# Performance work log

Measured on AMD Instinct MI355X. Metric: run time of the kernel, lower is better.

## Reference

```python
import jax, jax.numpy as jnp
import numpy as np

EMBED = 1024
HEADS = 16
HEAD_DIM = EMBED // HEADS


def setup_inputs() -> dict:
    key = jax.random.key(0)
    ks = jax.random.split(key, 5)
    x = jax.random.normal(ks[0], (4, 2048, EMBED), dtype=jnp.float32)
    s = 1.0 / np.sqrt(EMBED)
    W_qkv = jax.random.normal(ks[1], (EMBED, 3 * EMBED), dtype=jnp.float32) * s
    b_qkv = jnp.zeros((3 * EMBED,), dtype=jnp.float32)
    W_proj = jax.random.normal(ks[2], (EMBED, EMBED), dtype=jnp.float32) * s
    b_proj = jnp.zeros((EMBED,), dtype=jnp.float32)
    return {"x": x, "W_qkv": W_qkv, "b_qkv": b_qkv, "W_proj": W_proj, "b_proj": b_proj}


def reference(x, W_qkv, b_qkv, W_proj, b_proj):
    B, S, E = x.shape
    scale = 1.0 / np.sqrt(HEAD_DIM)
    qkv = x @ W_qkv + b_qkv                      # [B,S,3E]
    qkv = qkv.reshape(B, S, 3, HEADS, HEAD_DIM)
    q, k, v = qkv[:, :, 0], qkv[:, :, 1], qkv[:, :, 2]   # [B,S,H,D]
    scores = jnp.einsum('bshd,bthd->bhst', q, k) * scale  # [B,H,S,S]
    attn = jax.nn.softmax(scores, axis=-1)
    out = jnp.einsum('bhst,bthd->bshd', attn, v)          # [B,S,H,D]
    out = out.reshape(B, S, E)
    return out @ W_proj + b_proj
```

## Files before the change

kernel.cpp:

```cpp
#include <hip/hip_runtime.h>
#include <math.h>

#define EMBED 1024
#define HEADS 16
#define HD    64
#define SEQ   2048
#define BATCH 4
#define ROWS  (BATCH * SEQ)

typedef _Float16 f16;
typedef __attribute__((ext_vector_type(8))) _Float16 f16x8;
typedef __attribute__((ext_vector_type(4))) _Float16 f16x4;
typedef __attribute__((ext_vector_type(2))) _Float16 f16x2;
typedef __attribute__((ext_vector_type(4))) float    fx4;

typedef __attribute__((address_space(3))) char  lds_char;
typedef __attribute__((address_space(1))) const char glb_char;

#define SCALE_Q 0.18033688011112042f

#define BAR_LGKM()  asm volatile("s_waitcnt lgkmcnt(0)\n\ts_barrier" ::: "memory")
#define BAR_VM8()   asm volatile("s_waitcnt vmcnt(8)\n\ts_barrier" ::: "memory")
#define BAR_VM0()   asm volatile("s_waitcnt vmcnt(0)\n\ts_barrier" ::: "memory")

__global__ __launch_bounds__(256) void prep(const float* __restrict__ x,
                                            f16* __restrict__ x_h,
                                            const float* __restrict__ Wqkv,
                                            f16* __restrict__ Wqt,
                                            const float* __restrict__ Wproj,
                                            f16* __restrict__ Wpt) {
    const int blk = blockIdx.x;
    if (blk < 8192) {
        const int i = (blk * 256 + threadIdx.x) * 4;
        const float4 v = *(const float4*)(x + i);
        f16x4 o = {(f16)v.x, (f16)v.y, (f16)v.z, (f16)v.w};
        *(f16x4*)(x_h + i) = o;
        return;
    }
    __shared__ float t[32][33];
    const float* W;
    f16* Wt;
    int N, bx, by;
    if (blk < 8192 + 3072) {
        const int b2 = blk - 8192;
        W = Wqkv; Wt = Wqt; N = 3072; bx = b2 % 96; by = b2 / 96;
    } else {
        const int b2 = blk - 8192 - 3072;
        W = Wproj; Wt = Wpt; N = 1024; bx = b2 % 32; by = b2 / 32;
    }
    const int tx = threadIdx.x & 31, ty = threadIdx.x >> 5;
    const int k0 = by * 32, n0 = bx * 32;
    #pragma unroll
    for (int i = 0; i < 4; i++)
        t[ty + i * 8][tx] = W[(size_t)(k0 + ty + i * 8) * N + n0 + tx];
    __syncthreads();
    #pragma unroll
    for (int i = 0; i < 4; i++)
        Wt[(size_t)(n0 + ty + i * 8) * 1024 + k0 + tx] = (f16)t[tx][ty + i * 8];
}

template <int MODE>
__global__ __launch_bounds__(256) void gemm_f16k(const f16* __restrict__ A,
                                                 const f16* __restrict__ Bt,
                                                 const float* __restrict__ bias,
                                                 float* __restrict__ Cf,
                                                 f16* __restrict__ qH,
                                                 f16* __restrict__ kH,
                                                 f16* __restrict__ vT,
                                                 int M, int N, int K) {
    constexpr int TEL = 128 * 64;
    __shared__ alignas(16) f16 smem[4 * TEL];

    f16 (*As0)[64] = (f16(*)[64])(smem);
    f16 (*As1)[64] = (f16(*)[64])(smem + TEL);
    f16 (*Bs0)[64] = (f16(*)[64])(smem + 2 * TEL);
    f16 (*Bs1)[64] = (f16(*)[64])(smem + 3 * TEL);
    lds_char* a0b = (lds_char*)smem;
    lds_char* a1b = (lds_char*)smem + 2 * TEL;
    lds_char* b0b = (lds_char*)smem + 4 * TEL;
    lds_char* b1b = (lds_char*)smem + 6 * TEL;

    const int tid  = threadIdx.x;
    const int wave = tid >> 6;
    const int lane = tid & 63;
    const int quad = lane >> 4;
    const int l16  = lane & 15;

    const int nwg  = gridDim.x * gridDim.y;
    const int flat = blockIdx.y * gridDim.x + blockIdx.x;
    const int swz  = (flat & 7) * (nwg >> 3) + (flat >> 3);
    const int bx   = swz % gridDim.x;
    const int by   = swz / gridDim.x;
    const int m0   = by * 128;
    const int n0   = bx * 128;
    const int wm   = wave & 1;
    const int wn   = wave >> 1;

    fx4 acc[4][4];
    #pragma unroll
    for (int i = 0; i < 4; i++)
        #pragma unroll
        for (int j = 0; j < 4; j++)
            acc[i][j] = (fx4){0.f, 0.f, 0.f, 0.f};

    const int srow = lane >> 3;
    const int sjl  = ((lane & 7) ^ (srow & 7)) * 8;
    auto STAGE = [&](lds_char* asb, lds_char* bsb, int k0) {
        #pragma unroll
        for (int it = 0; it < 4; it++) {
            const int g = it * 4 + wave;
            const int r = g * 8 + srow;
            __builtin_amdgcn_global_load_lds(
                (glb_char*)(A + (size_t)(m0 + r) * K + k0 + sjl),
                asb + g * 1024, 16, 0, 0);
            __builtin_amdgcn_global_load_lds(
                (glb_char*)(Bt + (size_t)(n0 + r) * K + k0 + sjl),
                bsb + g * 1024, 16, 0, 0);
        }
    };

    const int NT = K >> 6;

    auto ITER = [&](f16 (*As)[64], f16 (*Bs)[64],
                    lds_char* asb, lds_char* bsb, int t) {
        f16x8 af0[4], af1[4], bf0[4], bf1[4];
        #pragma unroll
        for (int i = 0; i < 4; i++) {
            const int ra = wm * 64 + i * 16 + l16;
            const int rb = wn * 64 + i * 16 + l16;
            af0[i] = *(const f16x8*)&As[ra][((0 + quad) ^ (ra & 7)) * 8];
            af1[i] = *(const f16x8*)&As[ra][((4 + quad) ^ (ra & 7)) * 8];
            bf0[i] = *(const f16x8*)&Bs[rb][((0 + quad) ^ (rb & 7)) * 8];
            bf1[i] = *(const f16x8*)&Bs[rb][((4 + quad) ^ (rb & 7)) * 8];
        }
        BAR_LGKM();
        const bool more = (t + 2 < NT);
        if (more) STAGE(asb, bsb, (t + 2) * 64);
        __builtin_amdgcn_s_setprio(1);
        #pragma unroll
        for (int i = 0; i < 4; i++)
            #pragma unroll
            for (int j = 0; j < 4; j++) {
                acc[i][j] = __builtin_amdgcn_mfma_f32_16x16x32_f16(af0[i], bf0[j], acc[i][j], 0, 0, 0);
                acc[i][j] = __builtin_amdgcn_mfma_f32_16x16x32_f16(af1[i], bf1[j], acc[i][j], 0, 0, 0);
            }
        __builtin_amdgcn_s_setprio(0);
        if (more) BAR_VM8(); else BAR_VM0();
    };

    STAGE(a0b, b0b, 0);
    STAGE(a1b, b1b, 64);
    BAR_VM8();

    for (int t = 0; t < NT; t += 2) {
        ITER(As0, Bs0, a0b, b0b, t);
        ITER(As1, Bs1, a1b, b1b, t + 1);
    }

    const int region = (MODE == 1) ? (n0 >> 10) : 0;

    if (MODE == 1 && region == 2) {
        const int b  = m0 >> 11;
        const int s0 = m0 & 2047;
        #pragma unroll
        for (int i = 0; i < 4; i++) {
            #pragma unroll
            for (int j = 0; j < 4; j++) {
                const int nloc = wn * 64 + j * 16 + l16;
                const float bn = bias[n0 + nloc];
                #pragma unroll
                for (int r = 0; r < 4; r++) {
                    const int sloc = wm * 64 + i * 16 + quad * 4 + r;
                    const int sp   = (sloc & ~31) | ((sloc & 15) << 1) | ((sloc >> 4) & 1);
                    const int phys = (sp >> 3) ^ (nloc & 15);
                    smem[nloc * 128 + phys * 8 + (sp & 7)] = (f16)(acc[i][j][r] + bn);
                }
            }
        }
        __syncthreads();
        const int nl = tid >> 1;
        const int hf = tid & 1;
        const int np0 = n0 - 2048;
        f16* dst = vT + ((size_t)(b * 16 + ((np0 + nl) >> 6)) * HD + (nl & 63)) * SEQ
                      + s0 + hf * 64;
        #pragma unroll
        for (int ch = 0; ch < 8; ch++) {
            const int lc   = hf * 8 + ch;
            const int phys = lc ^ (nl & 15);
            const f16x8 v  = *(const f16x8*)&smem[nl * 128 + phys * 8];
            *(f16x8*)(dst + ch * 8) = v;
        }
        return;
    }

    #pragma unroll
    for (int i = 0; i < 4; i++) {
        const int mb = m0 + wm * 64 + i * 16 + quad * 4;
        #pragma unroll
        for (int j = 0; j < 4; j++) {
            const int n  = n0 + wn * 64 + j * 16 + l16;
            const float bn = bias[n];
            #pragma unroll
            for (int r = 0; r < 4; r++) {
                const int m = mb + r;
                const float v = acc[i][j][r] + bn;
                if (MODE == 0) {
                    Cf[(size_t)m * N + n] = v;
                } else {
                    const int b = m >> 11, s = m & 2047;
                    if (region == 0) {
                        qH[(size_t)m * EMBED + n] = (f16)(v * SCALE_Q);
                    } else {
                        const int np = n - 1024, hh = np >> 6, d = np & 63;
                        kH[(((size_t)(b * 16 + hh) * SEQ + s) << 6) + d] = (f16)v;
                    }
                }
            }
        }
    }
}

__global__ __launch_bounds__(256, 4) void attn_mfma(const f16* __restrict__ qH,
                                                    const f16* __restrict__ kH,
                                                    const f16* __restrict__ vT,
                                                    f16* __restrict__ ctx) {
    __shared__ alignas(16) f16 Ks[64 * 64];
    __shared__ alignas(16) f16 Vt[64 * 64];
    __shared__ alignas(16) f16 Pl[4][2][16 * 64];

    const int tid  = threadIdx.x;
    const int wave = tid >> 6;
    const int lane = tid & 63;
    const int quad = lane >> 4;
    const int l16  = lane & 15;

    const int bid = (int)blockIdx.x;
    const int swz = (bid & 7) * 128 + (bid >> 3);
    const int qb = swz & 15;
    const int bh = swz >> 4;
    const int h  = bh & 15;
    const int b  = bh >> 4;
    const int q0 = qb * 128 + wave * 32;

    const f16* kB = kH + (size_t)bh * SEQ * HD;
    const f16* vB = vT + (size_t)bh * HD * SEQ;

    f16x8 qf[2][2];
    #pragma unroll
    for (int s = 0; s < 2; s++) {
        const f16* qp = qH + (size_t)(b * SEQ + q0 + s * 16 + l16) * EMBED + h * HD;
        #pragma unroll
        for (int c = 0; c < 2; c++)
            qf[s][c] = *(const f16x8*)(qp + c * 32 + quad * 8);
    }

    fx4 o[2][4];
    fx4 ls[2];
    #pragma unroll
    for (int s = 0; s < 2; s++) {
        ls[s] = (fx4){0.f, 0.f, 0.f, 0.f};
        #pragma unroll
        for (int dc = 0; dc < 4; dc++)
            o[s][dc] = (fx4){0.f, 0.f, 0.f, 0.f};
    }

    f16x8 ones8;
    #pragma unroll
    for (int j = 0; j < 8; j++) ones8[j] = (f16)1.0f;

    lds_char* ksb = (lds_char*)&Ks[0];
    lds_char* vsb = (lds_char*)&Vt[0];

    auto STAGE_K = [&](int kb) {
        #pragma unroll
        for (int it = 0; it < 2; it++) {
            const int g  = wave * 2 + it;
            const int c  = g * 64 + lane;
            const int r  = c >> 3;
            const int jl = (c & 7) ^ (r & 7);
            __builtin_amdgcn_global_load_lds(
                (glb_char*)(kB + (size_t)(kb * 64 + r) * HD + jl * 8),
                ksb + g * 1024, 16, 0, 0);
        }
    };
    auto STAGE_V = [&](int kb) {
        #pragma unroll
        for (int it = 0; it < 2; it++) {
            const int g  = wave * 2 + it;
            const int c  = g * 64 + lane;
            const int r  = c >> 3;
            const int jl = (c & 7) ^ (r & 7);
            __builtin_amdgcn_global_load_lds(
                (glb_char*)(vB + (size_t)r * SEQ + kb * 64 + jl * 8),
                vsb + g * 1024, 16, 0, 0);
        }
    };

    STAGE_K(0);
    STAGE_V(0);
    __syncthreads();

    for (int kb = 0; kb < SEQ / 64; kb++) {
        fx4 st0[4], st1[4];
        __builtin_amdgcn_s_setprio(1);
        #pragma unroll
        for (int t = 0; t < 4; t++) {
            const int row = l16 + 16 * t;
            const f16x8 kt0 = *(const f16x8*)&Ks[(row * 8 + ((0 + quad) ^ (row & 7))) * 8];
            const f16x8 kt1 = *(const f16x8*)&Ks[(row * 8 + ((4 + quad) ^ (row & 7))) * 8];
            fx4 z = {0.f, 0.f, 0.f, 0.f};
            st0[t] = __builtin_amdgcn_mfma_f32_16x16x32_f16(qf[0][0], kt0, z, 0, 0, 0);
            st0[t] = __builtin_amdgcn_mfma_f32_16x16x32_f16(qf[0][1], kt1, st0[t], 0, 0, 0);
            st1[t] = __builtin_amdgcn_mfma_f32_16x16x32_f16(qf[1][0], kt0, z, 0, 0, 0);
            st1[t] = __builtin_amdgcn_mfma_f32_16x16x32_f16(qf[1][1], kt1, st1[t], 0, 0, 0);
        }
        __builtin_amdgcn_s_setprio(0);

        #pragma unroll
        for (int g = 0; g < 2; g++)
            #pragma unroll
            for (int r = 0; r < 4; r++) {
                const int row = quad * 4 + r;
                const int cc  = (g * 4 + (l16 >> 2)) ^ (row & 7);
                {
                    const float pa = __builtin_amdgcn_exp2f(st0[2 * g][r]);
                    const float pb = __builtin_amdgcn_exp2f(st0[2 * g + 1][r]);
                    const f16x2 pk = __builtin_bit_cast(f16x2, __builtin_amdgcn_cvt_pkrtz(pa, pb));
                    *(f16x2*)&Pl[wave][0][row * 64 + cc * 8 + (l16 & 3) * 2] = pk;
                }
                {
                    const float pa = __builtin_amdgcn_exp2f(st1[2 * g][r]);
                    const float pb = __builtin_amdgcn_exp2f(st1[2 * g + 1][r]);
                    const f16x2 pk = __builtin_bit_cast(f16x2, __builtin_amdgcn_cvt_pkrtz(pa, pb));
                    *(f16x2*)&Pl[wave][1][row * 64 + cc * 8 + (l16 & 3) * 2] = pk;
                }
            }

        __syncthreads();
        if (kb + 1 < SEQ / 64) STAGE_K(kb + 1);

        const f16x8 pf00 = *(const f16x8*)&Pl[wave][0][l16 * 64 + ((0 + quad) ^ (l16 & 7)) * 8];
        const f16x8 pf01 = *(const f16x8*)&Pl[wave][0][l16 * 64 + ((4 + quad) ^ (l16 & 7)) * 8];
        const f16x8 pf10 = *(const f16x8*)&Pl[wave][1][l16 * 64 + ((0 + quad) ^ (l16 & 7)) * 8];
        const f16x8 pf11 = *(const f16x8*)&Pl[wave][1][l16 * 64 + ((4 + quad) ^ (l16 & 7)) * 8];
        __builtin_amdgcn_s_setprio(1);
        #pragma unroll
        for (int dc = 0; dc < 4; dc++) {
            const int row = 16 * dc + l16;
            const f16x8 vf0 = *(const f16x8*)&Vt[(row * 8 + ((0 + quad) ^ (row & 7))) * 8];
            const f16x8 vf1 = *(const f16x8*)&Vt[(row * 8 + ((4 + quad) ^ (row & 7))) * 8];
            o[0][dc] = __builtin_amdgcn_mfma_f32_16x16x32_f16(pf00, vf0, o[0][dc], 0, 0, 0);
            o[0][dc] = __builtin_amdgcn_mfma_f32_16x16x32_f16(pf01, vf1, o[0][dc], 0, 0, 0);
            o[1][dc] = __builtin_amdgcn_mfma_f32_16x16x32_f16(pf10, vf0, o[1][dc], 0, 0, 0);
            o[1][dc] = __builtin_amdgcn_mfma_f32_16x16x32_f16(pf11, vf1, o[1][dc], 0, 0, 0);
        }
        ls[0] = __builtin_amdgcn_mfma_f32_16x16x32_f16(pf00, ones8, ls[0], 0, 0, 0);
        ls[0] = __builtin_amdgcn_mfma_f32_16x16x32_f16(pf01, ones8, ls[0], 0, 0, 0);
        ls[1] = __builtin_amdgcn_mfma_f32_16x16x32_f16(pf10, ones8, ls[1], 0, 0, 0);
        ls[1] = __builtin_amdgcn_mfma_f32_16x16x32_f16(pf11, ones8, ls[1], 0, 0, 0);
        __builtin_amdgcn_s_setprio(0);

        __syncthreads();
        if (kb + 1 < SEQ / 64) STAGE_V(kb + 1);
    }

    #pragma unroll
    for (int s = 0; s < 2; s++) {
        #pragma unroll
        for (int r = 0; r < 4; r++) {
            const float inv = 1.0f / ls[s][r];
            const int q = q0 + s * 16 + quad * 4 + r;
            f16* dst = ctx + (size_t)(b * SEQ + q) * EMBED + h * HD;
            #pragma unroll
            for (int dc = 0; dc < 4; dc++)
                dst[dc * 16 + l16] = (f16)(o[s][dc][r] * inv);
        }
    }
}

extern "C" void kernel_launch(void* const* d_in, const int* in_sizes, int n_in,
                              void* d_out, int out_size, void* d_ws, size_t ws_size,
                              hipStream_t stream) {
    const float* x     = (const float*)d_in[0];
    const float* Wqkv  = (const float*)d_in[1];
    const float* bqkv  = (const float*)d_in[2];
    const float* Wproj = (const float*)d_in[3];
    const float* bproj = (const float*)d_in[4];
    float* out = (float*)d_out;

    f16* x_h = (f16*)d_ws;
    f16* qHb = x_h + (size_t)ROWS * EMBED;
    f16* kHb = qHb + (size_t)ROWS * EMBED;
    f16* vTb = kHb + (size_t)ROWS * EMBED;
    f16* ctx = vTb + (size_t)ROWS * EMBED;
    f16* Wqt = ctx + (size_t)ROWS * EMBED;
    f16* Wpt = Wqt + (size_t)3 * EMBED * EMBED;

    prep<<<dim3(12288), dim3(256), 0, stream>>>(x, x_h, Wqkv, Wqt, Wproj, Wpt);

    gemm_f16k<1><<<dim3(3 * EMBED / 128, ROWS / 128), dim3(256), 0, stream>>>(
        x_h, Wqt, bqkv, nullptr, qHb, kHb, vTb, ROWS, 3 * EMBED, EMBED);

    attn_mfma<<<dim3(64 * 16), dim3(256), 0, stream>>>(qHb, kHb, vTb, ctx);

    gemm_f16k<0><<<dim3(EMBED / 128, ROWS / 128), dim3(256), 0, stream>>>(
        ctx, Wpt, bproj, out, nullptr, nullptr, nullptr, ROWS, EMBED, EMBED);
}
```

Before: 269.4 us.

## Double-buffer K/V tiles in LDS and drop one barrier per iteration

Splits the K and V shared tiles into ping-pong buffers. The next tile's K and V are now prefetched at the start of each iteration, while the current tiles are being consumed. The loop is unrolled by two so each iteration needs a single __syncthreads instead of two. The per-wave P scratch is halved and reused sequentially for the two 16-row query sub-tiles, which serializes their exp/store/load/MFMA phases. Total LDS per block rises, which could matter for occupancy at four blocks per CU.

```diff
diff --git a/kernel.cpp b/kernel.cpp
--- a/kernel.cpp
+++ b/kernel.cpp
@@ -224,9 +224,11 @@
                                                     const f16* __restrict__ kH,
                                                     const f16* __restrict__ vT,
                                                     f16* __restrict__ ctx) {
-    __shared__ alignas(16) f16 Ks[64 * 64];
-    __shared__ alignas(16) f16 Vt[64 * 64];
-    __shared__ alignas(16) f16 Pl[4][2][16 * 64];
+    __shared__ alignas(16) f16 Ks0[64 * 64];
+    __shared__ alignas(16) f16 Ks1[64 * 64];
+    __shared__ alignas(16) f16 Vt0[64 * 64];
+    __shared__ alignas(16) f16 Vt1[64 * 64];
+    __shared__ alignas(16) f16 Pl[4][16 * 64];
 
     const int tid  = threadIdx.x;
     const int wave = tid >> 6;
@@ -268,10 +270,12 @@
     #pragma unroll
     for (int j = 0; j < 8; j++) ones8[j] = (f16)1.0f;
 
-    lds_char* ksb = (lds_char*)&Ks[0];
-    lds_char* vsb = (lds_char*)&Vt[0];
-
-    auto STAGE_K = [&](int kb) {
+    lds_char* ks0b = (lds_char*)&Ks0[0];
+    lds_char* ks1b = (lds_char*)&Ks1[0];
+    lds_char* vt0b = (lds_char*)&Vt0[0];
+    lds_char* vt1b = (lds_char*)&Vt1[0];
+
+    auto STAGE_K = [&](int kb, lds_char* ksb) {
         #pragma unroll
         for (int it = 0; it < 2; it++) {
             const int g  = wave * 2 + it;
@@ -283,7 +287,7 @@
                 ksb + g * 1024, 16, 0, 0);
         }
     };
-    auto STAGE_V = [&](int kb) {
+    auto STAGE_V = [&](int kb, lds_char* vsb) {
         #pragma unroll
         for (int it = 0; it < 2; it++) {
             const int g  = wave * 2 + it;
@@ -296,18 +300,47 @@
         }
     };
 
-    STAGE_K(0);
-    STAGE_V(0);
-    __syncthreads();
-
-    for (int kb = 0; kb < SEQ / 64; kb++) {
+    auto PVS = [&](const fx4* st, fx4* osd, fx4& lss, const f16* VtC) {
+        #pragma unroll
+        for (int g = 0; g < 2; g++)
+            #pragma unroll
+            for (int r = 0; r < 4; r++) {
+                const int row = quad * 4 + r;
+                const int cc  = (g * 4 + (l16 >> 2)) ^ (row & 7);
+                const float pa = __builtin_amdgcn_exp2f(st[2 * g][r]);
+                const float pb = __builtin_amdgcn_exp2f(st[2 * g + 1][r]);
+                const f16x2 pk = __builtin_bit_cast(f16x2, __builtin_amdgcn_cvt_pkrtz(pa, pb));
+                *(f16x2*)&Pl[wave][row * 64 + cc * 8 + (l16 & 3) * 2] = pk;
+            }
+        const f16x8 pf0 = *(const f16x8*)&Pl[wave][l16 * 64 + ((0 + quad) ^ (l16 & 7)) * 8];
+        const f16x8 pf1 = *(const f16x8*)&Pl[wave][l16 * 64 + ((4 + quad) ^ (l16 & 7)) * 8];
+        __builtin_amdgcn_s_setprio(1);
+        #pragma unroll
+        for (int dc = 0; dc < 4; dc++) {
+            const int row = 16 * dc + l16;
+            const f16x8 vf0 = *(const f16x8*)&VtC[(row * 8 + ((0 + quad) ^ (row & 7))) * 8];
+            const f16x8 vf1 = *(const f16x8*)&VtC[(row * 8 + ((4 + quad) ^ (row & 7))) * 8];
+            osd[dc] = __builtin_amdgcn_mfma_f32_16x16x32_f16(pf0, vf0, osd[dc], 0, 0, 0);
+            osd[dc] = __builtin_amdgcn_mfma_f32_16x16x32_f16(pf1, vf1, osd[dc], 0, 0, 0);
+        }
+        lss = __builtin_amdgcn_mfma_f32_16x16x32_f16(pf0, ones8, lss, 0, 0, 0);
+        lss = __builtin_amdgcn_mfma_f32_16x16x32_f16(pf1, ones8, lss, 0, 0, 0);
+        __builtin_amdgcn_s_setprio(0);
+    };
+
+    auto BODY = [&](const f16* KsC, const f16* VtC,
+                    lds_char* nks, lds_char* nvt, int kb) {
+        if (kb + 1 < SEQ / 64) {
+            STAGE_K(kb + 1, nks);
+            STAGE_V(kb + 1, nvt);
+        }
         fx4 st0[4], st1[4];
         __builtin_amdgcn_s_setprio(1);
         #pragma unroll
         for (int t = 0; t < 4; t++) {
             const int row = l16 + 16 * t;
-            const f16x8 kt0 = *(const f16x8*)&Ks[(row * 8 + ((0 + quad) ^ (row & 7))) * 8];
-            const f16x8 kt1 = *(const f16x8*)&Ks[(row * 8 + ((4 + quad) ^ (row & 7))) * 8];
+            const f16x8 kt0 = *(const f16x8*)&KsC[(row * 8 + ((0 + quad) ^ (row & 7))) * 8];
+            const f16x8 kt1 = *(const f16x8*)&KsC[(row * 8 + ((4 + quad) ^ (row & 7))) * 8];
             fx4 z = {0.f, 0.f, 0.f, 0.f};
             st0[t] = __builtin_amdgcn_mfma_f32_16x16x32_f16(qf[0][0], kt0, z, 0, 0, 0);
             st0[t] = __builtin_amdgcn_mfma_f32_16x16x32_f16(qf[0][1], kt1, st0[t], 0, 0, 0);
@@ -315,53 +348,18 @@
             st1[t] = __builtin_amdgcn_mfma_f32_16x16x32_f16(qf[1][1], kt1, st1[t], 0, 0, 0);
         }
         __builtin_amdgcn_s_setprio(0);
-
-        #pragma unroll
-        for (int g = 0; g < 2; g++)
-            #pragma unroll
-            for (int r = 0; r < 4; r++) {
-                const int row = quad * 4 + r;
-                const int cc  = (g * 4 + (l16 >> 2)) ^ (row & 7);
-                {
-                    const float pa = __builtin_amdgcn_exp2f(st0[2 * g][r]);
-                    const float pb = __builtin_amdgcn_exp2f(st0[2 * g + 1][r]);
-                    const f16x2 pk = __builtin_bit_cast(f16x2, __builtin_amdgcn_cvt_pkrtz(pa, pb));
-                    *(f16x2*)&Pl[wave][0][row * 64 + cc * 8 + (l16 & 3) * 2] = pk;
-                }
-                {
-                    const float pa = __builtin_amdgcn_exp2f(st1[2 * g][r]);
-                    const float pb = __builtin_amdgcn_exp2f(st1[2 * g + 1][r]);
-                    const f16x2 pk = __builtin_bit_cast(f16x2, __builtin_amdgcn_cvt_pkrtz(pa, pb));
-                    *(f16x2*)&Pl[wave][1][row * 64 + cc * 8 + (l16 & 3) * 2] = pk;
-                }
-            }
-
+        PVS(st0, o[0], ls[0], VtC);
+        PVS(st1, o[1], ls[1], VtC);
         __syncthreads();
-        if (kb + 1 < SEQ / 64) STAGE_K(kb + 1);
-
-        const f16x8 pf00 = *(const f16x8*)&Pl[wave][0][l16 * 64 + ((0 + quad) ^ (l16 & 7)) * 8];
-        const f16x8 pf01 = *(const f16x8*)&Pl[wave][0][l16 * 64 + ((4 + quad) ^ (l16 & 7)) * 8];
-        const f16x8 pf10 = *(const f16x8*)&Pl[wave][1][l16 * 64 + ((0 + quad) ^ (l16 & 7)) * 8];
-        const f16x8 pf11 = *(const f16x8*)&Pl[wave][1][l16 * 64 + ((4 + quad) ^ (l16 & 7)) * 8];
-        __builtin_amdgcn_s_setprio(1);
-        #pragma unroll
-        for (int dc = 0; dc < 4; dc++) {
-            const int row = 16 * dc + l16;
-            const f16x8 vf0 = *(const f16x8*)&Vt[(row * 8 + ((0 + quad) ^ (row & 7))) * 8];
-            const f16x8 vf1 = *(const f16x8*)&Vt[(row * 8 + ((4 + quad) ^ (row & 7))) * 8];
-            o[0][dc] = __builtin_amdgcn_mfma_f32_16x16x32_f16(pf00, vf0, o[0][dc], 0, 0, 0);
-            o[0][dc] = __builtin_amdgcn_mfma_f32_16x16x32_f16(pf01, vf1, o[0][dc], 0, 0, 0);
-            o[1][dc] = __builtin_amdgcn_mfma_f32_16x16x32_f16(pf10, vf0, o[1][dc], 0, 0, 0);
-            o[1][dc] = __builtin_amdgcn_mfma_f32_16x16x32_f16(pf11, vf1, o[1][dc], 0, 0, 0);
-        }
-        ls[0] = __builtin_amdgcn_mfma_f32_16x16x32_f16(pf00, ones8, ls[0], 0, 0, 0);
-        ls[0] = __builtin_amdgcn_mfma_f32_16x16x32_f16(pf01, ones8, ls[0], 0, 0, 0);
-        ls[1] = __builtin_amdgcn_mfma_f32_16x16x32_f16(pf10, ones8, ls[1], 0, 0, 0);
-        ls[1] = __builtin_amdgcn_mfma_f32_16x16x32_f16(pf11, ones8, ls[1], 0, 0, 0);
-        __builtin_amdgcn_s_setprio(0);
-
-        __syncthreads();
-        if (kb + 1 < SEQ / 64) STAGE_V(kb + 1);
+    };
+
+    STAGE_K(0, ks0b);
+    STAGE_V(0, vt0b);
+    __syncthreads();
+
+    for (int kb = 0; kb < SEQ / 64; kb += 2) {
+        BODY(Ks0, Vt0, ks1b, vt1b, kb);
+        BODY(Ks1, Vt1, ks0b, vt0b, kb + 1);
     }
 
     #pragma unroll
```

Result: slower. 345.3 us (+28.2%).
